# Performance work log

Hardware: AMD Instinct MI355X
Metric: run time of the kernel (lower is better)

The kernel has to match this reference:

```python
import jax, jax.numpy as jnp
import numpy as np

N_NODES = 100000
N_DIM = 512
N_REL = 64
N_TRIPLES = 200000


def setup_inputs() -> dict:
    key = jax.random.key(0)
    k1, k2, k3, k4, k5, k6 = jax.random.split(key, 6)
    embeddings = jax.random.normal(k1, (N_NODES, N_DIM), dtype=jnp.float32)
    s_idx = jax.random.randint(k2, (N_TRIPLES,), 0, N_NODES)
    r_idx = jax.random.randint(k3, (N_TRIPLES,), 0, N_REL)
    o_idx = jax.random.randint(k4, (N_TRIPLES,), 0, N_NODES)
    triples = jnp.stack([s_idx, r_idx, o_idx], axis=0)  # [3, T]
    # per-relation Linear(2*n_dim, 1): weight [n_rel, 2*n_dim], bias [n_rel]
    limit = 1.0 / np.sqrt(2 * N_DIM)  # torch Linear default init range
    W = jax.random.uniform(k5, (N_REL, 2 * N_DIM), jnp.float32, -limit, limit)
    b = jax.random.uniform(k6, (N_REL,), jnp.float32, -limit, limit)
    return {"embeddings": embeddings, "W": W, "b": b, "triples": triples}


def reference(embeddings, W, b, triples):
    # Gather subject/object embeddings and relation ids.
    s = embeddings[triples[0]]          # [T, d]
    r = triples[1]                      # [T]
    o = embeddings[triples[2]]          # [T, d]
    # Linear over cat([s, o]) == dot(s, W_s[r]) + dot(o, W_o[r]) + b[r]
    Ws = W[:, :N_DIM]                   # [R, d]
    Wo = W[:, N_DIM:]                   # [R, d]
    score = (jnp.einsum('td,td->t', s, Ws[r])
             + jnp.einsum('td,td->t', o, Wo[r])
             + b[r])                    # [T]
    return score
```

## Files before the change

### kernel.cpp

```cpp
#include <hip/hip_runtime.h>
#include <hip/hip_bf16.h>


#define NDIM 512
#define NV4  (NDIM / 4)

__global__ __launch_bounds__(256) void kg_score_kernel(
    const float* __restrict__ emb,
    const float* __restrict__ W,
    const float* __restrict__ b,
    const int*   __restrict__ triples,
    float*       __restrict__ out,
    int T)
{
    const int wid  = (int)((blockIdx.x * (unsigned)blockDim.x + threadIdx.x) >> 6);
    const int lane = threadIdx.x & 63;
    if (wid >= T) return;

    const int s = triples[wid];
    const int r = triples[T + wid];
    const int o = triples[2 * T + wid];

    const float4* __restrict__ srow = (const float4*)(emb + (long)s * NDIM);
    const float4* __restrict__ orow = (const float4*)(emb + (long)o * NDIM);
    const float4* __restrict__ wsrow = (const float4*)(W + (long)r * (2 * NDIM));
    const float4* __restrict__ worow = wsrow + NV4;

    float acc = 0.0f;
#pragma unroll
    for (int k = 0; k < 2; ++k) {
        const int idx = lane + k * 64;
        float4 sv = srow[idx];
        float4 wv = wsrow[idx];
        acc = fmaf(sv.x, wv.x, acc);
        acc = fmaf(sv.y, wv.y, acc);
        acc = fmaf(sv.z, wv.z, acc);
        acc = fmaf(sv.w, wv.w, acc);
        float4 ov = orow[idx];
        float4 uv = worow[idx];
        acc = fmaf(ov.x, uv.x, acc);
        acc = fmaf(ov.y, uv.y, acc);
        acc = fmaf(ov.z, uv.z, acc);
        acc = fmaf(ov.w, uv.w, acc);
    }

#pragma unroll
    for (int off = 32; off > 0; off >>= 1)
        acc += __shfl_xor(acc, off, 64);

    if (lane == 0)
        out[wid] = acc + b[r];
}

extern "C" void kernel_launch(void* const* d_in, const int* in_sizes, int n_in,
                              void* d_out, int out_size, void* d_ws, size_t ws_size,
                              hipStream_t stream)
{
    const float* emb     = (const float*)d_in[0];
    const float* W       = (const float*)d_in[1];
    const float* b       = (const float*)d_in[2];
    const int*   triples = (const int*)d_in[3];
    float*       out     = (float*)d_out;

    const int T = in_sizes[3] / 3;

    const int block = 256;
    const int wavesPerBlock = block / 64;
    const int grid = (T + wavesPerBlock - 1) / wavesPerBlock;

    kg_score_kernel<<<grid, block, 0, stream>>>(emb, W, b, triples, out, T);
}
```

Measured before the change: 351.2 us.

## Precompute per-node relation projections via split-bf16 MFMA GEMM, then gather scores

Replaces the per-triple gather of two 512-float embedding rows with a dense projection. Every node embedding is multiplied by all 64 subject and 64 object weight vectors, giving P[M,128]. A small gather kernel then sums two entries of P plus the bias for each triple. The GEMM uses bf16 MFMA with hi/lo splitting (three products) to approximate fp32 accuracy, and each row of the table is read once instead of random 2KB row gathers per triple. In exchange it needs a ~51MB workspace, an extra weight-prep kernel and an extra launch, and falls back to the old kernel if the workspace is too small.

Result: no change. 355.2 us (+1.1%).

```diff
diff --git a/kernel.cpp b/kernel.cpp
--- a/kernel.cpp
+++ b/kernel.cpp
@@ -1,17 +1,126 @@
 #include <hip/hip_runtime.h>
 #include <hip/hip_bf16.h>
 
+#define NDIM 512
+#define NREL 64
+#define NCOL 128
+#define KSTEPS (NDIM / 32)
 
-#define NDIM 512
-#define NV4  (NDIM / 4)
+typedef float f32x4 __attribute__((ext_vector_type(4)));
+typedef short s16x8 __attribute__((ext_vector_type(8)));
+
+static __device__ __forceinline__ short f2bf_rne(float f) {
+    union { float f; unsigned u; } v; v.f = f;
+    unsigned u = v.u + 0x7fffu + ((v.u >> 16) & 1u);
+    return (short)(u >> 16);
+}
+static __device__ __forceinline__ float bf2f(short h) {
+    union { unsigned u; float f; } v;
+    v.u = ((unsigned)(unsigned short)h) << 16;
+    return v.f;
+}
+
+__global__ __launch_bounds__(256) void prep_B_kernel(
+    const float* __restrict__ W, short* __restrict__ Bh, short* __restrict__ Bl)
+{
+    const int t = blockIdx.x * 256 + threadIdx.x;
+    const int i  = t & 7;
+    const int l  = (t >> 3) & 63;
+    const int c  = (t >> 9) & 7;
+    const int ks = t >> 12;
+    const int k = ks * 32 + ((l >> 4) << 3) + i;
+    const int n = (c << 4) + (l & 15);
+    const float w = W[(n & 63) * (2 * NDIM) + (n >> 6) * NDIM + k];
+    const short hi = f2bf_rne(w);
+    const short lo = f2bf_rne(w - bf2f(hi));
+    Bh[t] = hi;
+    Bl[t] = lo;
+}
+
+__global__ __launch_bounds__(256) void gemm_proj_kernel(
+    const float* __restrict__ emb, const short* __restrict__ Bh,
+    const short* __restrict__ Bl, float* __restrict__ P, int M)
+{
+    const int lane = threadIdx.x & 63;
+    const int wave = threadIdx.x >> 6;
+    const int rbase = blockIdx.x * 128 + wave * 32;
+    const int rcol = lane & 15;
+    const int koff = (lane >> 4) << 3;
+
+    const long r0c = (long)min(rbase + rcol, M - 1) * NDIM;
+    const long r1c = (long)min(rbase + 16 + rcol, M - 1) * NDIM;
+
+    f32x4 acc[2][8];
+#pragma unroll
+    for (int f = 0; f < 2; ++f)
+#pragma unroll
+        for (int c = 0; c < 8; ++c)
+            acc[f][c] = (f32x4){0.f, 0.f, 0.f, 0.f};
+
+    for (int ks = 0; ks < KSTEPS; ++ks) {
+        const float* a0p = emb + r0c + ks * 32 + koff;
+        const float* a1p = emb + r1c + ks * 32 + koff;
+        f32x4 a0a = *(const f32x4*)(a0p);
+        f32x4 a0b = *(const f32x4*)(a0p + 4);
+        f32x4 a1a = *(const f32x4*)(a1p);
+        f32x4 a1b = *(const f32x4*)(a1p + 4);
+
+        s16x8 a0h, a0l, a1h, a1l;
+#pragma unroll
+        for (int j = 0; j < 4; ++j) {
+            short h;
+            h = f2bf_rne(a0a[j]); a0h[j]     = h; a0l[j]     = f2bf_rne(a0a[j] - bf2f(h));
+            h = f2bf_rne(a0b[j]); a0h[4 + j] = h; a0l[4 + j] = f2bf_rne(a0b[j] - bf2f(h));
+            h = f2bf_rne(a1a[j]); a1h[j]     = h; a1l[j]     = f2bf_rne(a1a[j] - bf2f(h));
+            h = f2bf_rne(a1b[j]); a1h[4 + j] = h; a1l[4 + j] = f2bf_rne(a1b[j] - bf2f(h));
+        }
+
+        const s16x8* bhp = (const s16x8*)(Bh) + (long)ks * 512 + lane;
+        const s16x8* blp = (const s16x8*)(Bl) + (long)ks * 512 + lane;
+#pragma unroll
+        for (int c = 0; c < 8; ++c) {
+            s16x8 bh = bhp[c * 64];
+            s16x8 bl = blp[c * 64];
+            acc[0][c] = __builtin_amdgcn_mfma_f32_16x16x32_bf16(a0h, bh, acc[0][c], 0, 0, 0);
+            acc[0][c] = __builtin_amdgcn_mfma_f32_16x16x32_bf16(a0l, bh, acc[0][c], 0, 0, 0);
+            acc[0][c] = __builtin_amdgcn_mfma_f32_16x16x32_bf16(a0h, bl, acc[0][c], 0, 0, 0);
+            acc[1][c] = __builtin_amdgcn_mfma_f32_16x16x32_bf16(a1h, bh, acc[1][c], 0, 0, 0);
+            acc[1][c] = __builtin_amdgcn_mfma_f32_16x16x32_bf16(a1l, bh, acc[1][c], 0, 0, 0);
+            acc[1][c] = __builtin_amdgcn_mfma_f32_16x16x32_bf16(a1h, bl, acc[1][c], 0, 0, 0);
+        }
+    }
+
+#pragma unroll
+    for (int f = 0; f < 2; ++f) {
+        const int rb = rbase + f * 16 + ((lane >> 4) << 2);
+#pragma unroll
+        for (int c = 0; c < 8; ++c) {
+#pragma unroll
+            for (int i = 0; i < 4; ++i) {
+                const int r = rb + i;
+                if (r < M)
+                    P[(long)r * NCOL + c * 16 + rcol] = acc[f][c][i];
+            }
+        }
+    }
+}
+
+__global__ __launch_bounds__(256) void gather_score_kernel(
+    const float* __restrict__ P, const float* __restrict__ b,
+    const int* __restrict__ triples, float* __restrict__ out, int T)
+{
+    const int t = blockIdx.x * 256 + threadIdx.x;
+    if (t >= T) return;
+    const int s = triples[t];
+    const int r = triples[T + t];
+    const int o = triples[2 * T + t];
+    out[t] = P[(long)s * NCOL + r] + P[(long)o * NCOL + NREL + r] + b[r];
+}
 
 __global__ __launch_bounds__(256) void kg_score_kernel(
-    const float* __restrict__ emb,
-    const float* __restrict__ W,
-    const float* __restrict__ b,
-    const int*   __restrict__ triples,
-    float*       __restrict__ out,
-    int T)
+    const float* __restrict__ emb, const float* __restrict__ W,
+    const float* __restrict__ b, const int* __restrict__ triples,
+    float* __restrict__ out, int T)
 {
     const int wid  = (int)((blockIdx.x * (unsigned)blockDim.x + threadIdx.x) >> 6);
     const int lane = threadIdx.x & 63;
@@ -21,10 +130,10 @@
     const int r = triples[T + wid];
     const int o = triples[2 * T + wid];
 
-    const float4* __restrict__ srow = (const float4*)(emb + (long)s * NDIM);
-    const float4* __restrict__ orow = (const float4*)(emb + (long)o * NDIM);
+    const float4* __restrict__ srow  = (const float4*)(emb + (long)s * NDIM);
+    const float4* __restrict__ orow  = (const float4*)(emb + (long)o * NDIM);
     const float4* __restrict__ wsrow = (const float4*)(W + (long)r * (2 * NDIM));
-    const float4* __restrict__ worow = wsrow + NV4;
+    const float4* __restrict__ worow = wsrow + NDIM / 4;
 
     float acc = 0.0f;
 #pragma unroll
@@ -32,22 +141,16 @@
         const int idx = lane + k * 64;
         float4 sv = srow[idx];
         float4 wv = wsrow[idx];
-        acc = fmaf(sv.x, wv.x, acc);
-        acc = fmaf(sv.y, wv.y, acc);
-        acc = fmaf(sv.z, wv.z, acc);
-        acc = fmaf(sv.w, wv.w, acc);
+        acc = fmaf(sv.x, wv.x, acc); acc = fmaf(sv.y, wv.y, acc);
+        acc = fmaf(sv.z, wv.z, acc); acc = fmaf(sv.w, wv.w, acc);
         float4 ov = orow[idx];
         float4 uv = worow[idx];
-        acc = fmaf(ov.x, uv.x, acc);
-        acc = fmaf(ov.y, uv.y, acc);
-        acc = fmaf(ov.z, uv.z, acc);
-        acc = fmaf(ov.w, uv.w, acc);
+        acc = fmaf(ov.x, uv.x, acc); acc = fmaf(ov.y, uv.y, acc);
+        acc = fmaf(ov.z, uv.z, acc); acc = fmaf(ov.w, uv.w, acc);
     }
-
 #pragma unroll
     for (int off = 32; off > 0; off >>= 1)
         acc += __shfl_xor(acc, off, 64);
-
     if (lane == 0)
         out[wid] = acc + b[r];
 }
@@ -62,11 +165,24 @@
     const int*   triples = (const int*)d_in[3];
     float*       out     = (float*)d_out;
 
+    const int M = in_sizes[0] / NDIM;
     const int T = in_sizes[3] / 3;
 
-    const int block = 256;
-    const int wavesPerBlock = block / 64;
-    const int grid = (T + wavesPerBlock - 1) / wavesPerBlock;
+    const size_t pBytes  = (size_t)M * NCOL * sizeof(float);
+    const size_t bBytes  = (size_t)NDIM * NCOL * sizeof(short);
+    const size_t need    = pBytes + 2 * bBytes;
 
-    kg_score_kernel<<<grid, block, 0, stream>>>(emb, W, b, triples, out, T);
+    if (ws_size >= need) {
+        float* P  = (float*)d_ws;
+        short* Bh = (short*)((char*)d_ws + pBytes);
+        short* Bl = Bh + (size_t)NDIM * NCOL;
+
+        prep_B_kernel<<<(NDIM * NCOL) / 256, 256, 0, stream>>>(W, Bh, Bl);
+        gemm_proj_kernel<<<(M + 127) / 128, 256, 0, stream>>>(emb, Bh, Bl, P, M);
+        gather_score_kernel<<<(T + 255) / 256, 256, 0, stream>>>(P, b, triples, out, T);
+    } else {
+        const int block = 256;
+        const int grid = (T + 3) / 4;
+        kg_score_kernel<<<grid, block, 0, stream>>>(emb, W, b, triples, out, T);
+    }
 }
```
